# Performance work log

Measured on AMD Instinct MI355X. Metric: run time of the kernel, lower is better.

Reference implementation:

```python
import jax, jax.numpy as jnp
import numpy as np
from jax import lax

STEP_SIZE = 0.1
T0, T1 = 0.0, 1.0
NUM_STEPS = int(abs(T1 - T0) / STEP_SIZE)  # 10 leapfrog steps

B = 65536
N_DIM = 128      # q and p each have N_DIM dims; x has 2*N_DIM
HIDDEN = 512


def setup_inputs() -> dict:
    key = jax.random.key(0)
    k_x, k_w1, k_w2 = jax.random.split(key, 3)
    x = jax.random.normal(k_x, (B, 2 * N_DIM), dtype=jnp.float32)
    # potential MLP: Linear(N_DIM, HIDDEN) -> tanh -> Linear(HIDDEN, 1)
    W1 = jax.random.normal(k_w1, (N_DIM, HIDDEN), dtype=jnp.float32) / np.sqrt(N_DIM)
    b1 = jnp.zeros((HIDDEN,), dtype=jnp.float32)
    W2 = jax.random.normal(k_w2, (HIDDEN, 1), dtype=jnp.float32) / np.sqrt(HIDDEN)
    b2 = jnp.zeros((1,), dtype=jnp.float32)
    return {"x": x, "W1": W1, "b1": b1, "W2": W2, "b2": b2}


def reference(x, W1, b1, W2, b2):
    """Symplectic (leapfrog-style) forward integration of the Hamiltonian ODE.

    H(q,p) = 0.5*sum(p^2) + V(q), V(q) = MLP(q) with scalar output.
    Per step (faithful to the torch loop, grads taken jointly at (q,p)):
        dH/dq = dV/dq,  dH/dp = p
        p <- p - dV/dq * dt
        q <- q + p_old * dt
    """
    dt = jnp.float32(STEP_SIZE)
    n = x.shape[-1] // 2
    q0, p0 = x[..., :n], x[..., n:]

    def V_sum(q):  # sum over batch of scalar potential
        h = jnp.tanh(q @ W1 + b1)          # [B, HIDDEN]
        v = (h @ W2)[..., 0] + b2[0]       # [B]
        return v.sum()

    grad_V = jax.grad(V_sum)  # [B, n] -> dV/dq per sample (sum decouples)

    def step(carry, _):
        q, p = carry
        dH_dq = grad_V(q)      # grads at (q, p_old)
        dH_dp = p
        p_new = p - dH_dq * dt
        q_new = q + dH_dp * dt
        return (q_new, p_new), None

    (qf, pf), _ = lax.scan(step, (q0, p0), None, length=NUM_STEPS)
    return jnp.concatenate([qf, pf], axis=-1)
```

## Files before the change

kernel.cpp:

```cpp
#include <hip/hip_runtime.h>
#include <hip/hip_bf16.h>

typedef float f32x4 __attribute__((ext_vector_type(4)));
typedef __bf16 bf16x8 __attribute__((ext_vector_type(8)));
typedef unsigned int u32;
typedef unsigned int u32x4 __attribute__((ext_vector_type(4)));

#if defined(__has_builtin)
#if __has_builtin(__builtin_amdgcn_exp2f)
#define EXP2F(x) __builtin_amdgcn_exp2f(x)
#else
#define EXP2F(x) exp2f(x)
#endif
#if __has_builtin(__builtin_amdgcn_rcpf)
#define RCPF(x) __builtin_amdgcn_rcpf(x)
#else
#define RCPF(x) (1.0f/(x))
#endif
#else
#define EXP2F(x) exp2f(x)
#define RCPF(x) (1.0f/(x))
#endif

#define MFMA16(a,b,c) __builtin_amdgcn_mfma_f32_16x16x32_bf16((a),(b),(c),0,0,0)

__device__ __forceinline__ unsigned short f2bf(float f) {
  return __builtin_bit_cast(unsigned short, (__bf16)f);
}

__device__ __forceinline__ u32 pkbf(float a, float b) {
  u32 d;
  asm("v_cvt_pk_bf16_f32 %0, %1, %2" : "=v"(d) : "v"(a), "v"(b));
  return d;
}

__global__ __launch_bounds__(256) void hn_prep(const float* __restrict__ W1,
                                               unsigned short* __restrict__ ws) {
  int t = blockIdx.x * 256 + threadIdx.x;
  int rho = t >> 7, io = t & 127;
  int j = (rho >> 5) * 32 + ((rho >> 2) & 3) * 8 + ((rho >> 4) & 1) * 4 + (rho & 3);
  int i = (io >> 5) * 32 + ((io >> 2) & 1) * 16 + ((io >> 3) & 3) * 4 + (io & 3);
  ws[t] = f2bf(W1[i * 512 + j]);
  ws[65536 + t] = f2bf(W1[t]);
}

__global__ __launch_bounds__(512, 2) void hn_main(
    const float* __restrict__ x, const float* __restrict__ W1,
    const float* __restrict__ b1, const float* __restrict__ W2,
    const unsigned short* __restrict__ wsp, float* __restrict__ out) {
  __shared__ __align__(16) char w1f[131072];
  __shared__ __align__(16) float b1s[512];
  __shared__ __align__(16) float w2s[512];

  const int tid = threadIdx.x;
  const int lane = tid & 63;
  const int w = tid >> 6;
  const int m = lane & 15;
  const int g = lane >> 4;

  for (int it = tid; it < 8192; it += 512) {
    int flat = it << 3;
    int rho = flat >> 7;
    u32x4 v = *(const u32x4*)(wsp + flat);
    int ba = flat << 1;
    *(u32x4*)(w1f + (ba ^ ((rho & 7) << 4))) = v;
  }
  if (tid < 512) {
    b1s[tid] = b1[tid] * 2.8853900817779268f;
    w2s[tid] = W2[tid];
  }
  __syncthreads();

  const int b0 = blockIdx.x * 256 + w * 32;

  float q[2][4][8], p[2][4][8];
#pragma unroll
  for (int bf = 0; bf < 2; ++bf)
#pragma unroll
    for (int kb = 0; kb < 4; ++kb) {
      const float* r0 = x + (long)(b0 + 16 * bf + m) * 256 + kb * 32 + g * 4;
#pragma unroll
      for (int h = 0; h < 2; ++h) {
        f32x4 qv = *(const f32x4*)(r0 + h * 16);
        f32x4 pv = *(const f32x4*)(r0 + h * 16 + 128);
#pragma unroll
        for (int rr = 0; rr < 4; ++rr) {
          q[bf][kb][4 * h + rr] = qv[rr];
          p[bf][kb][4 * h + rr] = pv[rr];
        }
      }
    }

  const int sw = (m & 7) << 4;
  const int lbF[4] = {
      (m * 256 + 0 * 64 + g * 16) ^ sw,
      (m * 256 + 1 * 64 + g * 16) ^ sw,
      (m * 256 + 2 * 64 + g * 16) ^ sw,
      (m * 256 + 3 * 64 + g * 16) ^ sw};
  const unsigned short* W1b = wsp + 65536;
  const char* bptr = (const char*)W1b + m * 1024 + g * 16;

#pragma unroll 1
  for (int step = 0; step < 10; ++step) {
    u32x4 qbw[2][4];
#pragma unroll
    for (int bf = 0; bf < 2; ++bf)
#pragma unroll
      for (int kb = 0; kb < 4; ++kb)
#pragma unroll
        for (int h = 0; h < 4; ++h)
          qbw[bf][kb][h] = pkbf(q[bf][kb][2 * h], q[bf][kb][2 * h + 1]);

    f32x4 gacc[2][8];
#pragma unroll
    for (int bf = 0; bf < 2; ++bf)
#pragma unroll
      for (int nf = 0; nf < 8; ++nf) gacc[bf][nf] = f32x4{0.f, 0.f, 0.f, 0.f};

#pragma unroll 2
    for (int jblk = 0; jblk < 16; ++jblk) {
      f32x4 z[2][2];
      z[0][0] = f32x4{0.f,0.f,0.f,0.f}; z[0][1] = f32x4{0.f,0.f,0.f,0.f};
      z[1][0] = f32x4{0.f,0.f,0.f,0.f}; z[1][1] = f32x4{0.f,0.f,0.f,0.f};
#pragma unroll
      for (int kb = 0; kb < 4; ++kb) {
        bf16x8 qb0 = __builtin_bit_cast(bf16x8, qbw[0][kb]);
        bf16x8 qb1 = __builtin_bit_cast(bf16x8, qbw[1][kb]);
        bf16x8 a0 = *(const bf16x8*)(w1f + lbF[kb] + jblk * 8192);
        bf16x8 a1 = *(const bf16x8*)(w1f + lbF[kb] + jblk * 8192 + 4096);
        z[0][0] = MFMA16(a0, qb0, z[0][0]);
        z[0][1] = MFMA16(a0, qb1, z[0][1]);
        z[1][0] = MFMA16(a1, qb0, z[1][0]);
        z[1][1] = MFMA16(a1, qb1, z[1][1]);
      }
      u32x4 sp0, sp1;
#pragma unroll
      for (int jf = 0; jf < 2; ++jf) {
        f32x4 b1v = *(const f32x4*)(b1s + jblk * 32 + g * 8 + jf * 4);
        f32x4 w2v = *(const f32x4*)(w2s + jblk * 32 + g * 8 + jf * 4);
#pragma unroll
        for (int bf = 0; bf < 2; ++bf) {
          const f32x4 zv = z[jf][bf];
          float sv[4];
#pragma unroll
          for (int rr = 0; rr < 4; ++rr) {
            float zz = fmaf(zv[rr], 2.8853900817779268f, b1v[rr]);
            float e = EXP2F(zz);
            float u = RCPF(e + 1.f);
            float th = fmaf(-2.f, u, 1.f);
            sv[rr] = fmaf(-th * th, w2v[rr], w2v[rr]);
          }
          u32 w0 = pkbf(sv[0], sv[1]);
          u32 w1p = pkbf(sv[2], sv[3]);
          if (bf == 0) { sp0[jf * 2] = w0; sp0[jf * 2 + 1] = w1p; }
          else         { sp1[jf * 2] = w0; sp1[jf * 2 + 1] = w1p; }
        }
      }
      bf16x8 sB0 = __builtin_bit_cast(bf16x8, sp0);
      bf16x8 sB1 = __builtin_bit_cast(bf16x8, sp1);
#pragma unroll
      for (int nf = 0; nf < 8; ++nf) {
        bf16x8 af = *(const bf16x8*)(bptr + nf * 16384 + jblk * 64);
        gacc[0][nf] = MFMA16(af, sB0, gacc[0][nf]);
        gacc[1][nf] = MFMA16(af, sB1, gacc[1][nf]);
      }
    }

#pragma unroll
    for (int bf = 0; bf < 2; ++bf)
#pragma unroll
      for (int kb = 0; kb < 4; ++kb)
#pragma unroll
        for (int r = 0; r < 8; ++r)
          q[bf][kb][r] = fmaf(0.1f, p[bf][kb][r], q[bf][kb][r]);

#pragma unroll
    for (int bf = 0; bf < 2; ++bf)
#pragma unroll
      for (int kb = 0; kb < 4; ++kb)
#pragma unroll
        for (int r = 0; r < 8; ++r)
          p[bf][kb][r] = fmaf(-0.1f, gacc[bf][2 * kb + (r >> 2)][r & 3], p[bf][kb][r]);
  }

#pragma unroll
  for (int bf = 0; bf < 2; ++bf)
#pragma unroll
    for (int kb = 0; kb < 4; ++kb) {
      float* o = out + (long)(b0 + 16 * bf + m) * 256 + kb * 32 + g * 4;
#pragma unroll
      for (int h = 0; h < 2; ++h) {
        f32x4 qv, pv;
#pragma unroll
        for (int rr = 0; rr < 4; ++rr) {
          qv[rr] = q[bf][kb][4 * h + rr];
          pv[rr] = p[bf][kb][4 * h + rr];
        }
        *(f32x4*)(o + h * 16) = qv;
        *(f32x4*)(o + h * 16 + 128) = pv;
      }
    }
}

extern "C" void kernel_launch(void* const* d_in, const int* in_sizes, int n_in,
                              void* d_out, int out_size, void* d_ws, size_t ws_size,
                              hipStream_t stream) {
  const float* x  = (const float*)d_in[0];
  const float* W1 = (const float*)d_in[1];
  const float* b1 = (const float*)d_in[2];
  const float* W2 = (const float*)d_in[3];
  float* out = (float*)d_out;
  unsigned short* wsp = (unsigned short*)d_ws;

  hipLaunchKernelGGL(hn_prep, dim3(256), dim3(256), 0, stream, W1, wsp);
  hipLaunchKernelGGL(hn_main, dim3(256), dim3(512), 0, stream,
                     x, W1, b1, W2, wsp, out);
}
```

Baseline: 351.4 us.

## Software-pipeline forward activation with backward fold and accumulate gradients directly into p

Restructures the hidden-block loop so that the forward matmul and tanh-derivative work for block j runs alongside the backward gradient MFMAs for block j-1, letting matrix and vector work interleave. It also removes the 64-register gacc accumulator: each backward MFMA starts from zero and its result is folded into p at once with the -dt scale. The q update now runs before the hidden loop, which is safe because p is updated only inside the fold. This cuts register pressure, but adds many more scalar FMAs and rounds each block's partial gradient separately. The jblk loop drops from unroll 2 to unroll 1.

```diff
diff --git a/kernel.cpp b/kernel.cpp
--- a/kernel.cpp
+++ b/kernel.cpp
@@ -100,9 +100,67 @@
   const unsigned short* W1b = wsp + 65536;
   const char* bptr = (const char*)W1b + m * 1024 + g * 16;
 
+  u32x4 qbw[2][4];
+
+  auto fwd_act = [&](int jblk, u32x4& so0, u32x4& so1) {
+    f32x4 z[2][2];
+    z[0][0] = f32x4{0.f,0.f,0.f,0.f}; z[0][1] = f32x4{0.f,0.f,0.f,0.f};
+    z[1][0] = f32x4{0.f,0.f,0.f,0.f}; z[1][1] = f32x4{0.f,0.f,0.f,0.f};
+#pragma unroll
+    for (int kb = 0; kb < 4; ++kb) {
+      bf16x8 qb0 = __builtin_bit_cast(bf16x8, qbw[0][kb]);
+      bf16x8 qb1 = __builtin_bit_cast(bf16x8, qbw[1][kb]);
+      bf16x8 a0 = *(const bf16x8*)(w1f + lbF[kb] + jblk * 8192);
+      bf16x8 a1 = *(const bf16x8*)(w1f + lbF[kb] + jblk * 8192 + 4096);
+      z[0][0] = MFMA16(a0, qb0, z[0][0]);
+      z[0][1] = MFMA16(a0, qb1, z[0][1]);
+      z[1][0] = MFMA16(a1, qb0, z[1][0]);
+      z[1][1] = MFMA16(a1, qb1, z[1][1]);
+    }
+#pragma unroll
+    for (int jf = 0; jf < 2; ++jf) {
+      f32x4 b1v = *(const f32x4*)(b1s + jblk * 32 + g * 8 + jf * 4);
+      f32x4 w2v = *(const f32x4*)(w2s + jblk * 32 + g * 8 + jf * 4);
+#pragma unroll
+      for (int bf = 0; bf < 2; ++bf) {
+        const f32x4 zv = z[jf][bf];
+        float sv[4];
+#pragma unroll
+        for (int rr = 0; rr < 4; ++rr) {
+          float zz = fmaf(zv[rr], 2.8853900817779268f, b1v[rr]);
+          float e = EXP2F(zz);
+          float u = RCPF(e + 1.f);
+          float th = fmaf(-2.f, u, 1.f);
+          sv[rr] = fmaf(-th * th, w2v[rr], w2v[rr]);
+        }
+        u32 w0 = pkbf(sv[0], sv[1]);
+        u32 w1p = pkbf(sv[2], sv[3]);
+        if (bf == 0) { so0[jf * 2] = w0; so0[jf * 2 + 1] = w1p; }
+        else         { so1[jf * 2] = w0; so1[jf * 2 + 1] = w1p; }
+      }
+    }
+  };
+
+  auto bwd_fold = [&](int jblk, u32x4 s0, u32x4 s1) {
+    bf16x8 sB0 = __builtin_bit_cast(bf16x8, s0);
+    bf16x8 sB1 = __builtin_bit_cast(bf16x8, s1);
+    const f32x4 zc = f32x4{0.f, 0.f, 0.f, 0.f};
+#pragma unroll
+    for (int nf = 0; nf < 8; ++nf) {
+      bf16x8 af = *(const bf16x8*)(bptr + nf * 16384 + jblk * 64);
+      f32x4 gt0 = MFMA16(af, sB0, zc);
+      f32x4 gt1 = MFMA16(af, sB1, zc);
+      const int kb = nf >> 1, h4 = (nf & 1) * 4;
+#pragma unroll
+      for (int rr = 0; rr < 4; ++rr) {
+        p[0][kb][h4 + rr] = fmaf(-0.1f, gt0[rr], p[0][kb][h4 + rr]);
+        p[1][kb][h4 + rr] = fmaf(-0.1f, gt1[rr], p[1][kb][h4 + rr]);
+      }
+    }
+  };
+
 #pragma unroll 1
   for (int step = 0; step < 10; ++step) {
-    u32x4 qbw[2][4];
 #pragma unroll
     for (int bf = 0; bf < 2; ++bf)
 #pragma unroll
@@ -111,61 +169,6 @@
         for (int h = 0; h < 4; ++h)
           qbw[bf][kb][h] = pkbf(q[bf][kb][2 * h], q[bf][kb][2 * h + 1]);
 
-    f32x4 gacc[2][8];
-#pragma unroll
-    for (int bf = 0; bf < 2; ++bf)
-#pragma unroll
-      for (int nf = 0; nf < 8; ++nf) gacc[bf][nf] = f32x4{0.f, 0.f, 0.f, 0.f};
-
-#pragma unroll 2
-    for (int jblk = 0; jblk < 16; ++jblk) {
-      f32x4 z[2][2];
-      z[0][0] = f32x4{0.f,0.f,0.f,0.f}; z[0][1] = f32x4{0.f,0.f,0.f,0.f};
-      z[1][0] = f32x4{0.f,0.f,0.f,0.f}; z[1][1] = f32x4{0.f,0.f,0.f,0.f};
-#pragma unroll
-      for (int kb = 0; kb < 4; ++kb) {
-        bf16x8 qb0 = __builtin_bit_cast(bf16x8, qbw[0][kb]);
-        bf16x8 qb1 = __builtin_bit_cast(bf16x8, qbw[1][kb]);
-        bf16x8 a0 = *(const bf16x8*)(w1f + lbF[kb] + jblk * 8192);
-        bf16x8 a1 = *(const bf16x8*)(w1f + lbF[kb] + jblk * 8192 + 4096);
-        z[0][0] = MFMA16(a0, qb0, z[0][0]);
-        z[0][1] = MFMA16(a0, qb1, z[0][1]);
-        z[1][0] = MFMA16(a1, qb0, z[1][0]);
-        z[1][1] = MFMA16(a1, qb1, z[1][1]);
-      }
-      u32x4 sp0, sp1;
-#pragma unroll
-      for (int jf = 0; jf < 2; ++jf) {
-        f32x4 b1v = *(const f32x4*)(b1s + jblk * 32 + g * 8 + jf * 4);
-        f32x4 w2v = *(const f32x4*)(w2s + jblk * 32 + g * 8 + jf * 4);
-#pragma unroll
-        for (int bf = 0; bf < 2; ++bf) {
-          const f32x4 zv = z[jf][bf];
-          float sv[4];
-#pragma unroll
-          for (int rr = 0; rr < 4; ++rr) {
-            float zz = fmaf(zv[rr], 2.8853900817779268f, b1v[rr]);
-            float e = EXP2F(zz);
-            float u = RCPF(e + 1.f);
-            float th = fmaf(-2.f, u, 1.f);
-            sv[rr] = fmaf(-th * th, w2v[rr], w2v[rr]);
-          }
-          u32 w0 = pkbf(sv[0], sv[1]);
-          u32 w1p = pkbf(sv[2], sv[3]);
-          if (bf == 0) { sp0[jf * 2] = w0; sp0[jf * 2 + 1] = w1p; }
-          else         { sp1[jf * 2] = w0; sp1[jf * 2 + 1] = w1p; }
-        }
-      }
-      bf16x8 sB0 = __builtin_bit_cast(bf16x8, sp0);
-      bf16x8 sB1 = __builtin_bit_cast(bf16x8, sp1);
-#pragma unroll
-      for (int nf = 0; nf < 8; ++nf) {
-        bf16x8 af = *(const bf16x8*)(bptr + nf * 16384 + jblk * 64);
-        gacc[0][nf] = MFMA16(af, sB0, gacc[0][nf]);
-        gacc[1][nf] = MFMA16(af, sB1, gacc[1][nf]);
-      }
-    }
-
 #pragma unroll
     for (int bf = 0; bf < 2; ++bf)
 #pragma unroll
@@ -174,13 +177,15 @@
         for (int r = 0; r < 8; ++r)
           q[bf][kb][r] = fmaf(0.1f, p[bf][kb][r], q[bf][kb][r]);
 
-#pragma unroll
-    for (int bf = 0; bf < 2; ++bf)
-#pragma unroll
-      for (int kb = 0; kb < 4; ++kb)
-#pragma unroll
-        for (int r = 0; r < 8; ++r)
-          p[bf][kb][r] = fmaf(-0.1f, gacc[bf][2 * kb + (r >> 2)][r & 3], p[bf][kb][r]);
+    u32x4 sA0, sA1, sC0, sC1;
+    fwd_act(0, sA0, sA1);
+#pragma unroll 1
+    for (int jblk = 1; jblk < 16; ++jblk) {
+      fwd_act(jblk, sC0, sC1);
+      bwd_fold(jblk - 1, sA0, sA1);
+      sA0 = sC0; sA1 = sC1;
+    }
+    bwd_fold(15, sA0, sA1);
   }
 
 #pragma unroll
```

Result: slower. 415.2 us (+18.1%).
